# Performance work log

Hardware: AMD Instinct MI355X
Metric: run time of the kernel (lower is better)

Reference implementation:

```python
import jax, jax.numpy as jnp
import numpy as np

NUM_SINK = 8  # cfg.SINKHORN_ITERS


def _sinkhorn_log(c, log_a, log_b, lambd):
    # c: [M+1, N+1] augmented coupling scores (sinkhorn_unrolled: log_p = -c/lambd)
    log_p = -c / lambd
    for _ in range(NUM_SINK):  # fixed small unroll, matches num_sink
        log_p = log_p - (jax.nn.logsumexp(log_p, axis=-2, keepdims=True) - log_b[None, :])
        log_p = log_p - (jax.nn.logsumexp(log_p, axis=-1, keepdims=True) - log_a[:, None])
    return jnp.exp(log_p)


def setup_inputs() -> dict:
    key = jax.random.key(0)
    k1, k2 = jax.random.split(key)
    G, M, N, D = 128, 512, 512, 512
    return {
        "det_feats": jax.random.normal(k1, (G, N, D), dtype=jnp.float32),
        "tra_feats": jax.random.normal(k2, (G, M, D), dtype=jnp.float32),
        "alpha": jnp.ones((1,), dtype=jnp.float32),
        "eplison": jnp.zeros((1,), dtype=jnp.float32),
    }


def reference(det_feats, tra_feats, alpha, eplison):
    G, N, D = det_feats.shape
    M = tra_feats.shape[1]
    # cosine affinity per graph: [G, M, N]
    corr = jnp.einsum('gmd,gnd->gmn', tra_feats, det_feats)
    n1 = jnp.linalg.norm(tra_feats, axis=-1)  # [G, M]
    n2 = jnp.linalg.norm(det_feats, axis=-1)  # [G, N]
    affinity = corr / (n1[:, :, None] * n2[:, None, :])
    a = alpha[0]
    bins0 = jnp.broadcast_to(a, (G, M, 1)).astype(affinity.dtype)
    bins1 = jnp.broadcast_to(a, (G, 1, N)).astype(affinity.dtype)
    corner = jnp.broadcast_to(a, (G, 1, 1)).astype(affinity.dtype)
    couplings = jnp.concatenate([
        jnp.concatenate([affinity, bins0], axis=-1),
        jnp.concatenate([bins1, corner], axis=-1),
    ], axis=-2)  # [G, M+1, N+1]
    norm = 1.0 / (M + N)
    a_aug = jnp.full((M + 1,), norm, dtype=jnp.float32).at[-1].set(norm * N)
    b_aug = jnp.full((N + 1,), norm, dtype=jnp.float32).at[-1].set(norm * M)
    log_a = jnp.log(a_aug)
    log_b = jnp.log(b_aug)
    lambd = jnp.exp(eplison[0]) + 0.03
    pred = jax.vmap(lambda c: _sinkhorn_log(c, log_a, log_b, lambd))(couplings)
    return pred  # [G, M+1, N+1]
```

## Files before the change

### kernel.cpp

```cpp
#include <hip/hip_runtime.h>
#include <hip/hip_bf16.h>

#define G    128
#define MDIM 512
#define NDIM 512
#define DDIM 512
#define NORMC 0.0009765625f
#define BINW  0.5f
#define PW   516

using short8 = __attribute__((ext_vector_type(8))) short;
using short4v = __attribute__((ext_vector_type(4))) short;
using f32x4 = __attribute__((ext_vector_type(4))) float;

__device__ inline float bf2f(unsigned short u) {
    unsigned int x = ((unsigned int)u) << 16;
    return __builtin_bit_cast(float, x);
}
__device__ inline unsigned short f2bf(float f) {
    return __builtin_bit_cast(unsigned short, __float2bfloat16(f));
}
__device__ inline short4v cvt4(float4 f) {
    short4v r;
    r[0] = __builtin_bit_cast(short, __float2bfloat16(f.x));
    r[1] = __builtin_bit_cast(short, __float2bfloat16(f.y));
    r[2] = __builtin_bit_cast(short, __float2bfloat16(f.z));
    r[3] = __builtin_bit_cast(short, __float2bfloat16(f.w));
    return r;
}
__device__ inline unsigned char f2e4m3(float f) {
    unsigned int b = __builtin_bit_cast(unsigned int, f);
    unsigned int t = b + 0x7FFFFu + ((b >> 20) & 1u);
    return (unsigned char)((t >> 20) - 960u);
}
__device__ inline float e4m32f(unsigned int u) {
    return __builtin_bit_cast(float, (u << 20) + 0x3C000000u);
}

__global__ __launch_bounds__(256)
void gt_cvt_kernel(const float* __restrict__ tra, const float* __restrict__ det,
                   unsigned short* __restrict__ trab, unsigned short* __restrict__ detb)
{
    int wave = threadIdx.x >> 6, lane = threadIdx.x & 63;
    long row0 = (long)blockIdx.x * 8 + wave * 2;
    const long per = (long)G * MDIM;
    const float* src; unsigned short* dst; long r0;
    if (row0 < per) { src = tra; dst = trab; r0 = row0; }
    else            { src = det; dst = detb; r0 = row0 - per; }
    const float4* p0 = reinterpret_cast<const float4*>(src + r0 * DDIM);
    const float4* p1 = reinterpret_cast<const float4*>(src + (r0 + 1) * DDIM);
    float4 a0 = p0[lane * 2], a1 = p0[lane * 2 + 1];
    float4 b0 = p1[lane * 2], b1 = p1[lane * 2 + 1];
    float sa = a0.x*a0.x + a0.y*a0.y + a0.z*a0.z + a0.w*a0.w
             + a1.x*a1.x + a1.y*a1.y + a1.z*a1.z + a1.w*a1.w;
    float sb = b0.x*b0.x + b0.y*b0.y + b0.z*b0.z + b0.w*b0.w
             + b1.x*b1.x + b1.y*b1.y + b1.z*b1.z + b1.w*b1.w;
    #pragma unroll
    for (int off = 1; off < 64; off <<= 1) {
        sa += __shfl_xor(sa, off);
        sb += __shfl_xor(sb, off);
    }
    float ra = rsqrtf(sa), rb = rsqrtf(sb);
    short8 oa, ob;
    {
        short4v lo = cvt4(make_float4(a0.x*ra, a0.y*ra, a0.z*ra, a0.w*ra));
        short4v hi = cvt4(make_float4(a1.x*ra, a1.y*ra, a1.z*ra, a1.w*ra));
        oa[0]=lo[0]; oa[1]=lo[1]; oa[2]=lo[2]; oa[3]=lo[3];
        oa[4]=hi[0]; oa[5]=hi[1]; oa[6]=hi[2]; oa[7]=hi[3];
    }
    {
        short4v lo = cvt4(make_float4(b0.x*rb, b0.y*rb, b0.z*rb, b0.w*rb));
        short4v hi = cvt4(make_float4(b1.x*rb, b1.y*rb, b1.z*rb, b1.w*rb));
        ob[0]=lo[0]; ob[1]=lo[1]; ob[2]=lo[2]; ob[3]=lo[3];
        ob[4]=hi[0]; ob[5]=hi[1]; ob[6]=hi[2]; ob[7]=hi[3];
    }
    *reinterpret_cast<short8*>(dst + (size_t)r0 * 512 + lane * 8)       = oa;
    *reinterpret_cast<short8*>(dst + (size_t)(r0 + 1) * 512 + lane * 8) = ob;
}

__global__ __launch_bounds__(256)
void gt_gemm_bf16(const unsigned short* __restrict__ trab, const unsigned short* __restrict__ detb,
                  const float* __restrict__ eps,
                  unsigned char* __restrict__ Ke, float* __restrict__ P1)
{
    __shared__ short As[128 * 40];
    __shared__ short Bs[128 * 40];
    int bid = blockIdx.x;
    int xcd = bid & 7, slot = bid >> 3;
    int g = xcd * 16 + (slot >> 4);
    int tile = slot & 15;
    int tm = tile >> 2, tn = tile & 3;
    int t = threadIdx.x, lane = t & 63, wave = t >> 6;
    int wr = wave >> 1, wc = wave & 1;
    f32x4 acc[4][4] = {};
    const unsigned short* Ab = trab + ((size_t)g << 18) + (size_t)(tm * 128) * 512;
    const unsigned short* Bb = detb + ((size_t)g << 18) + (size_t)(tn * 128) * 512;
    int srow = t >> 2;
    int sslot = t & 3;

    for (int kt = 0; kt < 16; ++kt) {
        int k0 = kt * 32;
        #pragma unroll
        for (int p = 0; p < 2; ++p) {
            int row = p * 64 + srow;
            short8 a = *reinterpret_cast<const short8*>(Ab + (size_t)row * 512 + k0 + sslot * 8);
            short8 b = *reinterpret_cast<const short8*>(Bb + (size_t)row * 512 + k0 + sslot * 8);
            *reinterpret_cast<short8*>(&As[row * 40 + sslot * 8]) = a;
            *reinterpret_cast<short8*>(&Bs[row * 40 + sslot * 8]) = b;
        }
        __syncthreads();
        short8 af[4], bfv[4];
        #pragma unroll
        for (int i = 0; i < 4; ++i) {
            int arow = wr * 64 + i * 16 + (lane & 15);
            af[i]  = *reinterpret_cast<const short8*>(&As[arow * 40 + (lane >> 4) * 8]);
            int brow = wc * 64 + i * 16 + (lane & 15);
            bfv[i] = *reinterpret_cast<const short8*>(&Bs[brow * 40 + (lane >> 4) * 8]);
        }
        #pragma unroll
        for (int i = 0; i < 4; ++i)
            #pragma unroll
            for (int j = 0; j < 4; ++j)
                acc[i][j] = __builtin_amdgcn_mfma_f32_16x16x32_bf16(af[i], bfv[j], acc[i][j], 0, 0, 0);
        __syncthreads();
    }

    float lam = __expf(eps[0]) + 0.03f;
    float nscale = -1.0f / lam;
    size_t kbase = (size_t)g << 18;
    int r0v = (lane >> 4) * 4;
    int c0 = lane & 15;
    #pragma unroll
    for (int j = 0; j < 4; ++j) {
        int lcol = wc * 64 + j * 16 + c0;
        int colg = tn * 128 + lcol;
        float cacc = 0.f;
        #pragma unroll
        for (int i = 0; i < 4; ++i) {
            int lrow = wr * 64 + i * 16 + r0v;
            #pragma unroll
            for (int r = 0; r < 4; ++r) {
                float ev = __expf(acc[i][j][r] * nscale);
                unsigned char q = f2e4m3(ev);
                Ke[kbase + (size_t)(tm * 128 + lrow + r) * 512 + colg] = q;
                cacc += e4m32f(q);
            }
        }
        cacc += __shfl_down(cacc, 32);
        cacc += __shfl_down(cacc, 16);
        if (lane < 16)
            P1[(size_t)g * (8 * PW) + (size_t)(2 * tm + wr) * PW + tn * 128 + wc * 64 + j * 16 + lane] = cacc;
    }
}

__global__ __launch_bounds__(256)
void gt_gemm_legacy(const float* __restrict__ tra, const float* __restrict__ det,
                    const float* __restrict__ eps,
                    float* __restrict__ Koutf, float* __restrict__ P1)
{
    __shared__ short As[128 * 40];
    __shared__ short Bs[128 * 40];
    __shared__ float rnA[128];
    __shared__ float rnB[128];
    int bid = blockIdx.x;
    int xcd = bid & 7, slot = bid >> 3;
    int g = xcd * 16 + (slot >> 4);
    int tile = slot & 15;
    int tm = tile >> 2, tn = tile & 3;
    int t = threadIdx.x, lane = t & 63, wave = t >> 6;
    int wr = wave >> 1, wc = wave & 1;
    f32x4 acc[4][4] = {};
    const float* Abase = tra + (size_t)g * MDIM * DDIM + (size_t)(tm * 128) * DDIM;
    const float* Bbase = det + (size_t)g * NDIM * DDIM + (size_t)(tn * 128) * DDIM;
    int srow = t >> 3, scol = t & 7;
    float ssA[4] = {0.f, 0.f, 0.f, 0.f};
    float ssB[4] = {0.f, 0.f, 0.f, 0.f};

    for (int kt = 0; kt < 16; ++kt) {
        int k0 = kt * 32;
        #pragma unroll
        for (int p = 0; p < 4; ++p) {
            int row = p * 32 + srow;
            float4 a = *reinterpret_cast<const float4*>(Abase + (size_t)row * DDIM + k0 + scol * 4);
            float4 b = *reinterpret_cast<const float4*>(Bbase + (size_t)row * DDIM + k0 + scol * 4);
            ssA[p] += a.x*a.x + a.y*a.y + a.z*a.z + a.w*a.w;
            ssB[p] += b.x*b.x + b.y*b.y + b.z*b.z + b.w*b.w;
            *reinterpret_cast<short4v*>(&As[row * 40 + scol * 4]) = cvt4(a);
            *reinterpret_cast<short4v*>(&Bs[row * 40 + scol * 4]) = cvt4(b);
        }
        __syncthreads();
        short8 af[4], bfv[4];
        #pragma unroll
        for (int i = 0; i < 4; ++i) {
            int arow = wr * 64 + i * 16 + (lane & 15);
            af[i]  = *reinterpret_cast<const short8*>(&As[arow * 40 + (lane >> 4) * 8]);
            int brow = wc * 64 + i * 16 + (lane & 15);
            bfv[i] = *reinterpret_cast<const short8*>(&Bs[brow * 40 + (lane >> 4) * 8]);
        }
        #pragma unroll
        for (int i = 0; i < 4; ++i)
            #pragma unroll
            for (int j = 0; j < 4; ++j)
                acc[i][j] = __builtin_amdgcn_mfma_f32_16x16x32_bf16(af[i], bfv[j], acc[i][j], 0, 0, 0);
        __syncthreads();
    }

    #pragma unroll
    for (int p = 0; p < 4; ++p) {
        float a = ssA[p], b = ssB[p];
        a += __shfl_xor(a, 1); a += __shfl_xor(a, 2); a += __shfl_xor(a, 4);
        b += __shfl_xor(b, 1); b += __shfl_xor(b, 2); b += __shfl_xor(b, 4);
        if (scol == 0) { rnA[p * 32 + srow] = rsqrtf(a); rnB[p * 32 + srow] = rsqrtf(b); }
    }
    __syncthreads();

    float lam = __expf(eps[0]) + 0.03f;
    float nscale = -1.0f / lam;
    size_t obase = (size_t)g * 263169;
    int r0v = (lane >> 4) * 4;
    int c0 = lane & 15;
    #pragma unroll
    for (int j = 0; j < 4; ++j) {
        int lcol = wc * 64 + j * 16 + c0;
        int colg = tn * 128 + lcol;
        float sc2 = nscale * rnB[lcol];
        float cacc = 0.f;
        #pragma unroll
        for (int i = 0; i < 4; ++i) {
            int lrow = wr * 64 + i * 16 + r0v;
            #pragma unroll
            for (int r = 0; r < 4; ++r) {
                float ev = __expf(acc[i][j][r] * rnA[lrow + r] * sc2);
                cacc += ev;
                int rowg = tm * 128 + lrow + r;
                Koutf[obase + (size_t)rowg * 513 + colg] = ev;
            }
        }
        cacc += __shfl_down(cacc, 32);
        cacc += __shfl_down(cacc, 16);
        if (lane < 16)
            P1[(size_t)g * (8 * PW) + (size_t)(2 * tm + wr) * PW + tn * 128 + wc * 64 + j * 16 + lane] = cacc;
    }
}

template<bool FP8, bool LAST>
__global__ __launch_bounds__(512)
void gt_iter(const void* __restrict__ Kv,
             const float* __restrict__ alpha, const float* __restrict__ eps,
             const float* __restrict__ Pread, float* __restrict__ Pwrite,
             float* __restrict__ outp, int first, int writeP)
{
    __shared__ float bv_s[512];
    __shared__ float colpart[8][512];
    __shared__ float rtmp[8];
    __shared__ float scal[2];
    int g = blockIdx.y, rb = blockIdx.x;
    int t = threadIdx.x, lane = t & 63, wv = t >> 6;
    float lam = __expf(eps[0]) + 0.03f;
    float val = __expf(-alpha[0] / lam);
    const float* Pg = Pread + (size_t)g * (8 * PW);
    float au512p = first ? 1.0f : Pg[513];
    float cs = 0.f;
    #pragma unroll
    for (int b = 0; b < 8; ++b) cs += Pg[b * PW + t];
    float bvt = NORMC / (cs + val * au512p);
    bv_s[t] = bvt;
    float sb = bvt;
    #pragma unroll
    for (int off = 1; off < 64; off <<= 1) sb += __shfl_xor(sb, off);
    if (lane == 0) rtmp[wv] = sb;
    __syncthreads();
    if (t == 0) {
        float S_bv = 0.f;
        #pragma unroll
        for (int w = 0; w < 8; ++w) S_bv += rtmp[w];
        float S_au_prev;
        if (first) S_au_prev = 513.f;
        else { float s = 0.f; for (int b = 0; b < 8; ++b) s += Pg[b * PW + 512]; S_au_prev = s + au512p; }
        float bv512 = BINW / (val * S_au_prev);
        float au512n = BINW / (val * (S_bv + bv512));
        scal[0] = bv512;
        scal[1] = au512n;
        if (!LAST && rb == 0) Pwrite[(size_t)g * (8 * PW) + 513] = au512n;
    }
    __syncthreads();
    float bv512 = scal[0];

    float bvr[8];
    #pragma unroll
    for (int k = 0; k < 8; ++k) bvr[k] = bv_s[lane * 8 + k];
    float colacc[8] = {};
    float suma = 0.f;
    size_t base = FP8 ? ((size_t)g << 18) : ((size_t)g * 263169);
    size_t obase = (size_t)g * 263169;
    int rowbase = rb * 64;
    for (int rr = wv; rr < 64; rr += 8) {
        int r = rowbase + rr;
        float kv[8];
        if constexpr (FP8) {
            uint2 w = *reinterpret_cast<const uint2*>((const unsigned char*)Kv + base + (size_t)r * 512 + lane * 8);
            kv[0] = e4m32f(w.x & 255u);
            kv[1] = e4m32f((w.x >> 8) & 255u);
            kv[2] = e4m32f((w.x >> 16) & 255u);
            kv[3] = e4m32f(w.x >> 24);
            kv[4] = e4m32f(w.y & 255u);
            kv[5] = e4m32f((w.y >> 8) & 255u);
            kv[6] = e4m32f((w.y >> 16) & 255u);
            kv[7] = e4m32f(w.y >> 24);
        } else {
            const float* p = (const float*)Kv + base + (size_t)r * 513 + lane * 8;
            #pragma unroll
            for (int k = 0; k < 8; ++k) kv[k] = p[k];
        }
        float dot = 0.f;
        #pragma unroll
        for (int k = 0; k < 8; ++k) dot += kv[k] * bvr[k];
        #pragma unroll
        for (int off = 1; off < 64; off <<= 1) dot += __shfl_xor(dot, off);
        float au_r = NORMC / (dot + val * bv512);
        if constexpr (LAST) {
            float* orow = outp + obase + (size_t)r * 513;
            f32x4 o0, o1;
            #pragma unroll
            for (int k = 0; k < 4; ++k) {
                o0[k] = kv[k] * au_r * bvr[k];
                o1[k] = kv[4 + k] * au_r * bvr[4 + k];
            }
            *reinterpret_cast<f32x4*>(orow + lane * 8)     = o0;
            *reinterpret_cast<f32x4*>(orow + lane * 8 + 4) = o1;
            if (lane == 0) orow[512] = val * au_r * bv512;
        } else {
            suma += au_r;
            #pragma unroll
            for (int k = 0; k < 8; ++k) colacc[k] += kv[k] * au_r;
        }
    }
    if constexpr (LAST) {
        if (rb == 7) {
            float au512n = scal[1];
            float* brow = outp + obase + (size_t)512 * 513;
            brow[t] = val * au512n * bv_s[t];
            if (t == 0) brow[512] = val * au512n * bv512;
        }
    } else if (writeP) {
        #pragma unroll
        for (int k = 0; k < 8; ++k) colpart[wv][lane * 8 + k] = colacc[k];
        if (lane == 0) rtmp[wv] = suma;
        __syncthreads();
        float s0 = 0.f;
        #pragma unroll
        for (int w = 0; w < 8; ++w) s0 += colpart[w][t];
        float* Pw = Pwrite + (size_t)g * (8 * PW) + (size_t)rb * PW;
        Pw[t] = s0;
        if (t == 0) {
            float ss = 0.f;
            #pragma unroll
            for (int w = 0; w < 8; ++w) ss += rtmp[w];
            Pw[512] = ss;
        }
    }
}

extern "C" void kernel_launch(void* const* d_in, const int* in_sizes, int n_in,
                              void* d_out, int out_size, void* d_ws, size_t ws_size,
                              hipStream_t stream) {
    const float* det   = (const float*)d_in[0];
    const float* tra   = (const float*)d_in[1];
    const float* alpha = (const float*)d_in[2];
    const float* eps   = (const float*)d_in[3];
    float* out = (float*)d_out;

    float* P0 = (float*)d_ws;
    float* P1 = P0 + (size_t)G * 8 * PW;
    unsigned char* ke = (unsigned char*)(P1 + (size_t)G * 8 * PW);

    size_t smallBytes = (size_t)2 * G * 8 * PW * 4;
    bool fast = ws_size >= smallBytes + ((size_t)G << 18);

    if (fast) {
        unsigned short* trab = (unsigned short*)out;
        unsigned short* detb = trab + ((size_t)G << 18);
        gt_cvt_kernel<<<(2 * G * MDIM) / 8, 256, 0, stream>>>(tra, det, trab, detb);
        gt_gemm_bf16<<<2048, 256, 0, stream>>>(trab, detb, eps, ke, P1);
        float* Pr = P1; float* Pw = P0;
        for (int it = 0; it < 7; ++it) {
            gt_iter<true, false><<<dim3(8, G), 512, 0, stream>>>((const void*)ke, alpha, eps, Pr, Pw, nullptr, it == 0 ? 1 : 0, 1);
            float* tmp = Pr; Pr = Pw; Pw = tmp;
        }
        gt_iter<true, true><<<dim3(8, G), 512, 0, stream>>>((const void*)ke, alpha, eps, Pr, Pw, out, 0, 0);
    } else {
        gt_gemm_legacy<<<2048, 256, 0, stream>>>(tra, det, eps, out, P1);
        float* Pr = P1; float* Pw = P0;
        for (int it = 0; it < 7; ++it) {
            gt_iter<false, false><<<dim3(8, G), 512, 0, stream>>>((const void*)out, alpha, eps, Pr, Pw, nullptr, it == 0 ? 1 : 0, 1);
            float* tmp = Pr; Pr = Pw; Pw = tmp;
        }
        gt_iter<false, true><<<dim3(8, G), 512, 0, stream>>>((const void*)out, alpha, eps, Pr, Pw, out, 0, 0);
    }
}
```

Before: 273.3 us.

## Fuse Sinkhorn iterations into one cooperative kernel with fp8 kernel held in LDS

Replaces the eight per-iteration gt_iter launches with a single cooperative kernel of 256 blocks. Each block loads half of one graph's fp8 Gibbs kernel (128 KB) into shared memory once and runs all iterations from there, exchanging column partial sums through global memory with grid.sync between iterations. This removes repeated global reads of the kernel matrix and the per-iteration launch overhead. In exchange it needs about 150 KB of LDS per block, one block per CU, and a cooperative launch that must fit all 256 blocks at once, with a fallback to the old path if the launch fails.

```diff
diff --git a/kernel.cpp b/kernel.cpp
--- a/kernel.cpp
+++ b/kernel.cpp
@@ -1,5 +1,8 @@
 #include <hip/hip_runtime.h>
 #include <hip/hip_bf16.h>
+#include <hip/hip_cooperative_groups.h>
+
+namespace cg = cooperative_groups;
 
 #define G    128
 #define MDIM 512
@@ -243,6 +246,160 @@
     }
 }
 
+__global__ __launch_bounds__(512, 1)
+void gt_sink_coop(const unsigned char* __restrict__ Ke,
+                  const float* __restrict__ alpha, const float* __restrict__ eps,
+                  const float* __restrict__ P1init, float* __restrict__ Pex,
+                  float* __restrict__ outp)
+{
+    extern __shared__ char smem[];
+    unsigned char* Ksh = (unsigned char*)smem;
+    float* bv_s    = (float*)(smem + 131072);
+    float* colpart = bv_s + 512;
+    float* rtmp    = colpart + 8 * 512;
+    float* scal    = rtmp + 8;
+
+    cg::grid_group grid = cg::this_grid();
+    int bid = blockIdx.x;
+    int g = bid >> 1, b = bid & 1;
+    int t = threadIdx.x, lane = t & 63, wv = t >> 6;
+    float lam = __expf(eps[0]) + 0.03f;
+    float val = __expf(-alpha[0] / lam);
+
+    {
+        const uint4* src = reinterpret_cast<const uint4*>(Ke + ((size_t)g << 18) + ((size_t)b << 17));
+        uint4* dst = reinterpret_cast<uint4*>(Ksh);
+        #pragma unroll
+        for (int i = 0; i < 16; ++i) dst[t + 512 * i] = src[t + 512 * i];
+    }
+    __syncthreads();
+
+    float au512p = 1.0f;
+    float* PexG = Pex + (size_t)g * (8 * PW);
+    size_t obase = (size_t)g * 263169;
+
+    for (int it = 0; it < 8; ++it) {
+        float cs;
+        if (it == 0) {
+            const float* Pg = P1init + (size_t)g * (8 * PW);
+            cs = 0.f;
+            #pragma unroll
+            for (int k8 = 0; k8 < 8; ++k8) cs += Pg[k8 * PW + t];
+        } else {
+            int pr = (it - 1) & 1;
+            cs = PexG[(pr * 2 + 0) * PW + t] + PexG[(pr * 2 + 1) * PW + t];
+        }
+        float bvt = NORMC / (cs + val * au512p);
+        bv_s[t] = bvt;
+        float sbv = bvt;
+        #pragma unroll
+        for (int off = 1; off < 64; off <<= 1) sbv += __shfl_xor(sbv, off);
+        if (lane == 0) rtmp[wv] = sbv;
+        __syncthreads();
+        if (t == 0) {
+            float S_bv = 0.f;
+            #pragma unroll
+            for (int w = 0; w < 8; ++w) S_bv += rtmp[w];
+            float Sau;
+            if (it == 0) Sau = 513.f;
+            else {
+                int pr = (it - 1) & 1;
+                Sau = PexG[(pr * 2 + 0) * PW + 512] + PexG[(pr * 2 + 1) * PW + 512] + au512p;
+            }
+            float bv512 = BINW / (val * Sau);
+            scal[0] = bv512;
+            scal[1] = BINW / (val * (S_bv + bv512));
+        }
+        __syncthreads();
+        float bv512 = scal[0];
+        float au512n = scal[1];
+
+        float bvr[8];
+        #pragma unroll
+        for (int k = 0; k < 8; ++k) bvr[k] = bv_s[lane * 8 + k];
+
+        if (it < 7) {
+            float colacc[8] = {};
+            float suma = 0.f;
+            for (int i = 0; i < 32; ++i) {
+                int rl = wv + i * 8;
+                uint2 w = *reinterpret_cast<const uint2*>(Ksh + rl * 512 + lane * 8);
+                float kv[8];
+                kv[0] = e4m32f(w.x & 255u);
+                kv[1] = e4m32f((w.x >> 8) & 255u);
+                kv[2] = e4m32f((w.x >> 16) & 255u);
+                kv[3] = e4m32f(w.x >> 24);
+                kv[4] = e4m32f(w.y & 255u);
+                kv[5] = e4m32f((w.y >> 8) & 255u);
+                kv[6] = e4m32f((w.y >> 16) & 255u);
+                kv[7] = e4m32f(w.y >> 24);
+                float dot = 0.f;
+                #pragma unroll
+                for (int k = 0; k < 8; ++k) dot += kv[k] * bvr[k];
+                #pragma unroll
+                for (int off = 1; off < 64; off <<= 1) dot += __shfl_xor(dot, off);
+                float au_r = NORMC / (dot + val * bv512);
+                suma += au_r;
+                #pragma unroll
+                for (int k = 0; k < 8; ++k) colacc[k] += kv[k] * au_r;
+            }
+            #pragma unroll
+            for (int k = 0; k < 8; ++k) colpart[wv * 512 + lane * 8 + k] = colacc[k];
+            if (lane == 0) rtmp[wv] = suma;
+            __syncthreads();
+            float* Pw = PexG + ((it & 1) * 2 + b) * PW;
+            float s0 = 0.f;
+            #pragma unroll
+            for (int w = 0; w < 8; ++w) s0 += colpart[w * 512 + t];
+            Pw[t] = s0;
+            if (t == 0) {
+                float ss = 0.f;
+                #pragma unroll
+                for (int w = 0; w < 8; ++w) ss += rtmp[w];
+                Pw[512] = ss;
+            }
+            au512p = au512n;
+            grid.sync();
+        } else {
+            for (int i = 0; i < 32; ++i) {
+                int rl = wv + i * 8;
+                int r = b * 256 + rl;
+                uint2 w = *reinterpret_cast<const uint2*>(Ksh + rl * 512 + lane * 8);
+                float kv[8];
+                kv[0] = e4m32f(w.x & 255u);
+                kv[1] = e4m32f((w.x >> 8) & 255u);
+                kv[2] = e4m32f((w.x >> 16) & 255u);
+                kv[3] = e4m32f(w.x >> 24);
+                kv[4] = e4m32f(w.y & 255u);
+                kv[5] = e4m32f((w.y >> 8) & 255u);
+                kv[6] = e4m32f((w.y >> 16) & 255u);
+                kv[7] = e4m32f(w.y >> 24);
+                float dot = 0.f;
+                #pragma unroll
+                for (int k = 0; k < 8; ++k) dot += kv[k] * bvr[k];
+                #pragma unroll
+                for (int off = 1; off < 64; off <<= 1) dot += __shfl_xor(dot, off);
+                float au_r = NORMC / (dot + val * bv512);
+                float* orow = outp + obase + (size_t)r * 513;
+                f32x4 o0, o1;
+                #pragma unroll
+                for (int k = 0; k < 4; ++k) {
+                    o0[k] = kv[k] * au_r * bvr[k];
+                    o1[k] = kv[4 + k] * au_r * bvr[4 + k];
+                }
+                *reinterpret_cast<f32x4*>(orow + lane * 8)     = o0;
+                *reinterpret_cast<f32x4*>(orow + lane * 8 + 4) = o1;
+                if (lane == 0) orow[512] = val * au_r * bv512;
+            }
+            if (b == 1) {
+                float* brow = outp + obase + (size_t)512 * 513;
+                brow[t] = val * au512n * bv_s[t];
+                if (t == 0) brow[512] = val * au512n * bv512;
+            }
+        }
+    }
+}
+
 template<bool FP8, bool LAST>
 __global__ __launch_bounds__(512)
 void gt_iter(const void* __restrict__ Kv,
@@ -382,12 +539,28 @@
         unsigned short* detb = trab + ((size_t)G << 18);
         gt_cvt_kernel<<<(2 * G * MDIM) / 8, 256, 0, stream>>>(tra, det, trab, detb);
         gt_gemm_bf16<<<2048, 256, 0, stream>>>(trab, detb, eps, ke, P1);
-        float* Pr = P1; float* Pw = P0;
-        for (int it = 0; it < 7; ++it) {
-            gt_iter<true, false><<<dim3(8, G), 512, 0, stream>>>((const void*)ke, alpha, eps, Pr, Pw, nullptr, it == 0 ? 1 : 0, 1);
-            float* tmp = Pr; Pr = Pw; Pw = tmp;
-        }
-        gt_iter<true, true><<<dim3(8, G), 512, 0, stream>>>((const void*)ke, alpha, eps, Pr, Pw, out, 0, 0);
+
+        const unsigned int SMEM = 131072u + 512u * 4 + 8u * 512 * 4 + 8u * 4 + 2u * 4;
+        bool coop_ok = false;
+        if (hipFuncSetAttribute((const void*)gt_sink_coop,
+                                hipFuncAttributeMaxDynamicSharedMemorySize,
+                                (int)SMEM) == hipSuccess) {
+            const unsigned char* keArg = ke;
+            void* args[] = { (void*)&keArg, (void*)&alpha, (void*)&eps,
+                             (void*)&P1, (void*)&P0, (void*)&out };
+            if (hipLaunchCooperativeKernel((const void*)gt_sink_coop,
+                                           dim3(256), dim3(512),
+                                           args, SMEM, stream) == hipSuccess)
+                coop_ok = true;
+        }
+        if (!coop_ok) {
+            float* Pr = P1; float* Pw = P0;
+            for (int it = 0; it < 7; ++it) {
+                gt_iter<true, false><<<dim3(8, G), 512, 0, stream>>>((const void*)ke, alpha, eps, Pr, Pw, nullptr, it == 0 ? 1 : 0, 1);
+                float* tmp = Pr; Pr = Pw; Pw = tmp;
+            }
+            gt_iter<true, true><<<dim3(8, G), 512, 0, stream>>>((const void*)ke, alpha, eps, Pr, Pw, out, 0, 0);
+        }
     } else {
         gt_gemm_legacy<<<2048, 256, 0, stream>>>(tra, det, eps, out, P1);
         float* Pr = P1; float* Pw = P0;
```

After: 488.7 us. +78.8%, slower.
